# Performance work log

Hardware: AMD Instinct MI355X
Metric: run time of the kernel (lower is better)

Reference implementation:

```python
import jax, jax.numpy as jnp
import numpy as np

N_ATOMS = 20000
N_EDGES = 200000
C = 64
N_BASIS = 8
R_CUT = 5.0
NORM_FACTOR = 10.0
EPS = 1e-6
# coupling paths (in_way, r_way, out_way) with out = in + r - 2k, all ways <= 2
# index: 0:(0,0,0) 1:(0,1,1) 2:(0,2,2) 3:(1,0,1) 4:(1,1,0) 5:(1,1,2) 6:(1,2,1) 7:(2,0,2) 8:(2,1,1) 9:(2,2,0) 10:(2,2,2)
N_COMBO = 11


def setup_inputs() -> dict:
    key = jax.random.key(0)
    ks = jax.random.split(key, 16)
    f32 = jnp.float32
    return {
        "node0": jax.random.normal(ks[0], (N_ATOMS, C), f32),
        "node1": jax.random.normal(ks[1], (N_ATOMS, C, 3), f32),
        "node2": jax.random.normal(ks[2], (N_ATOMS, C, 3, 3), f32),
        "edge0": jax.random.normal(ks[3], (N_EDGES, C), f32),
        "rij": jax.random.normal(ks[4], (N_EDGES, 3), f32),
        "idx_i": jax.random.randint(ks[5], (N_EDGES,), 0, N_ATOMS),
        "idx_j": jax.random.randint(ks[6], (N_EDGES,), 0, N_ATOMS),
        "rbf_w": jax.random.normal(ks[7], (N_COMBO, N_BASIS, C), f32) * 0.1,
        "si_w0": jax.random.normal(ks[8], (C, C), f32) / np.sqrt(C),
        "si_b0": jnp.zeros((C,), f32),
        "si_w1": jax.random.normal(ks[9], (C, C), f32) / np.sqrt(C),
        "si_w2": jax.random.normal(ks[10], (C, C), f32) / np.sqrt(C),
        "nl_w1": jax.random.normal(ks[11], (C,), f32) * 0.1,
        "nl_b1": jnp.zeros((C,), f32),
        "nl_w2": jax.random.normal(ks[12], (C,), f32) * 0.1,
        "nl_b2": jnp.zeros((C,), f32),
    }


def reference(node0, node1, node2, edge0, rij, rbf_w, si_w0, si_b0, si_w1, si_w2,
              nl_w1, nl_b1, nl_w2, nl_b2, idx_i, idx_j):
    # ---- radial filters: Gaussian RBF * cosine cutoff, mixed per coupling path ----
    d = jnp.linalg.norm(rij, axis=-1)                         # [E]
    rhat = rij / (d[:, None] + 1e-12)                          # [E,3]
    mu = jnp.linspace(0.0, R_CUT, N_BASIS)
    g = jnp.exp(-2.0 * (d[:, None] - mu) ** 2)                 # [E,B]
    fcut = 0.5 * (jnp.cos(jnp.pi * jnp.clip(d, 0.0, R_CUT) / R_CUT) + 1.0)
    rbf = g * fcut[:, None]                                    # [E,B]
    fc = jnp.einsum('eb,kbc->kec', rbf, rbf_w)                 # [K,E,C]
    # ---- filter tensors of r_way 1,2 (outer products of unit vector) ----
    T1 = rhat                                                  # [E,3]
    T2 = rhat[:, :, None] * rhat[:, None, :]                   # [E,3,3]
    # ---- GraphConvLayer (conv_mode='node_j'): gather neighbor features ----
    h0 = node0[idx_j]                                          # [E,C]
    h1 = node1[idx_j]                                          # [E,C,3]
    h2 = node2[idx_j]                                          # [E,C,3,3]
    m0 = (fc[0] * h0
          + fc[4] * jnp.einsum('ecx,ex->ec', h1, T1)
          + fc[9] * jnp.einsum('ecxy,exy->ec', h2, T2))
    m1 = (fc[1][:, :, None] * (h0[:, :, None] * T1[:, None, :])
          + fc[3][:, :, None] * h1
          + fc[6][:, :, None] * jnp.einsum('ecx,exy->ecy', h1, T2)
          + fc[8][:, :, None] * jnp.einsum('ecxy,ey->ecx', h2, T1))
    m2 = (fc[2][:, :, None, None] * (h0[:, :, None, None] * T2[:, None])
          + fc[5][:, :, None, None] * (h1[:, :, :, None] * T1[:, None, None, :])
          + fc[7][:, :, None, None] * h2
          + fc[10][:, :, None, None] * jnp.einsum('ecxy,eyz->ecxz', h2, T2))
    # ---- per-way scatter_add over idx_i, normalized ----
    n = node0.shape[0]
    a0 = jax.ops.segment_sum(m0, idx_i, num_segments=n) / NORM_FACTOR
    a1 = jax.ops.segment_sum(m1, idx_i, num_segments=n) / NORM_FACTOR
    a2 = jax.ops.segment_sum(m2, idx_i, num_segments=n) / NORM_FACTOR
    # ---- SelfInteractionLayer: per-way channel mixing (bias only for way 0) ----
    s0 = a0 @ si_w0 + si_b0
    s1 = jnp.einsum('ncx,cd->ndx', a1, si_w1)
    s2 = jnp.einsum('ncxy,cd->ndxy', a2, si_w2)
    # ---- NonLinearLayer: silu on scalars, norm-gated silu on higher ways ----
    r0 = jax.nn.silu(s0)
    nrm1 = jnp.sqrt(jnp.sum(s1 * s1, axis=-1) + EPS)
    r1 = s1 * jax.nn.silu(nrm1 * nl_w1 + nl_b1)[:, :, None]
    nrm2 = jnp.sqrt(jnp.sum(s2 * s2, axis=(-2, -1)) + EPS)
    r2 = s2 * jax.nn.silu(nrm2 * nl_w2 + nl_b2)[:, :, None, None]
    # ---- res_add with node_info; update_edge=False -> edge_info unchanged ----
    return (node0 + r0, node1 + r1, node2 + r2, edge0)
```

## Files before the change

### kernel.cpp

```cpp
#include <hip/hip_runtime.h>
#include <math.h>

#define N_ATOMS 20000
#define N_EDGES 200000
#define CH 64
#define NB 8
#define NK 11
#define COPY_BLOCKS 12500

__global__ __launch_bounds__(256) void hist_kernel(
    const int* __restrict__ idx_i, int* __restrict__ counts)
{
    int e = blockIdx.x * blockDim.x + threadIdx.x;
    if (e >= N_EDGES) return;
    atomicAdd(&counts[idx_i[e]], 1);
}

__global__ __launch_bounds__(1024) void scan_kernel(
    const int* __restrict__ counts, int* __restrict__ offsets,
    int* __restrict__ cursor)
{
    __shared__ int part[1024];
    const int CHUNK = 20;
    int t = threadIdx.x;
    int beg = t * CHUNK;
    int s = 0;
    for (int k = 0; k < CHUNK; ++k) {
        int idx = beg + k;
        if (idx < N_ATOMS) s += counts[idx];
    }
    part[t] = s;
    __syncthreads();
    for (int off = 1; off < 1024; off <<= 1) {
        int v = (t >= off) ? part[t - off] : 0;
        __syncthreads();
        part[t] += v;
        __syncthreads();
    }
    int run = part[t] - s;
    for (int k = 0; k < CHUNK; ++k) {
        int idx = beg + k;
        if (idx < N_ATOMS) {
            offsets[idx] = run;
            cursor[idx] = run;
            run += counts[idx];
        }
    }
    if (t == 0) offsets[N_ATOMS] = N_EDGES;
}

__global__ __launch_bounds__(256) void scatter_geom_kernel(
    const float* __restrict__ rij, const int* __restrict__ idx_i,
    const int* __restrict__ idx_j, int* __restrict__ cursor,
    int* __restrict__ jlist, float4* __restrict__ ge4)
{
    int e = blockIdx.x * blockDim.x + threadIdx.x;
    if (e >= N_EDGES) return;

    float rx = rij[e * 3 + 0];
    float ry = rij[e * 3 + 1];
    float rz = rij[e * 3 + 2];
    float d = sqrtf(rx * rx + ry * ry + rz * rz);
    float inv = 1.0f / (d + 1e-12f);

    float dc = fminf(d, 5.0f);
    float fcut = 0.5f * (cosf(3.14159265358979323846f * dc * 0.2f) + 1.0f);

    float rbf[NB];
#pragma unroll
    for (int b = 0; b < NB; ++b) {
        float mu = (5.0f / 7.0f) * (float)b;
        float t = d - mu;
        rbf[b] = expf(-2.0f * t * t) * fcut;
    }

    int p = atomicAdd(&cursor[idx_i[e]], 1);
    jlist[p] = idx_j[e];
    ge4[p * 3 + 0] = make_float4(rx * inv, ry * inv, rz * inv, rbf[0]);
    ge4[p * 3 + 1] = make_float4(rbf[1], rbf[2], rbf[3], rbf[4]);
    ge4[p * 3 + 2] = make_float4(rbf[5], rbf[6], rbf[7], 0.f);
}

__global__ __launch_bounds__(64, 2) void atom_fused_kernel(
    const float* __restrict__ node0, const float* __restrict__ node1,
    const float* __restrict__ node2,
    const int* __restrict__ jlist, const int* __restrict__ offsets,
    const float4* __restrict__ ge4, const float* __restrict__ rbf_w,
    const float* __restrict__ si_w0, const float* __restrict__ si_b0,
    const float* __restrict__ si_w1, const float* __restrict__ si_w2,
    const float* __restrict__ nl_w1, const float* __restrict__ nl_b1,
    const float* __restrict__ nl_w2, const float* __restrict__ nl_b2,
    float* __restrict__ out0, float* __restrict__ out1, float* __restrict__ out2,
    const float4* __restrict__ edge0_in, float4* __restrict__ edge0_out)
{
    int n = blockIdx.x;
    int c = threadIdx.x;

    if (n >= N_ATOMS) {
        int cb = n - N_ATOMS;
        size_t base = (size_t)cb * 256;
#pragma unroll
        for (int k = 0; k < 4; ++k)
            edge0_out[base + k * 64 + c] = edge0_in[base + k * 64 + c];
        return;
    }

    __shared__ float abuf[CH][13];

    float wreg[NK * NB];
#pragma unroll
    for (int kb = 0; kb < NK * NB; ++kb) wreg[kb] = rbf_w[kb * CH + c];

    float a0 = 0.f;
    float a1[3] = {0.f, 0.f, 0.f};
    float a2[9] = {0.f, 0.f, 0.f, 0.f, 0.f, 0.f, 0.f, 0.f, 0.f};

    int beg = offsets[n];
    int end = offsets[n + 1];

    float4 g0, g1v, g2v;
    float h0 = 0.f, h1[3] = {0.f, 0.f, 0.f};
    float h2[9] = {0.f, 0.f, 0.f, 0.f, 0.f, 0.f, 0.f, 0.f, 0.f};
    int jnx = 0;

    if (beg < end) {
        int j = jlist[beg];
        g0 = ge4[beg * 3 + 0];
        g1v = ge4[beg * 3 + 1];
        g2v = ge4[beg * 3 + 2];
        h0 = node0[(size_t)j * CH + c];
#pragma unroll
        for (int x = 0; x < 3; ++x) h1[x] = node1[((size_t)j * CH + c) * 3 + x];
#pragma unroll
        for (int q = 0; q < 9; ++q) h2[q] = node2[((size_t)j * CH + c) * 9 + q];
        jnx = (beg + 1 < end) ? jlist[beg + 1] : 0;
    }

    for (int p = beg; p < end; ++p) {
        float rh[3] = {g0.x, g0.y, g0.z};
        float rbf[NB] = {g0.w, g1v.x, g1v.y, g1v.z, g1v.w, g2v.x, g2v.y, g2v.z};
        float ch0 = h0;
        float ch1[3] = {h1[0], h1[1], h1[2]};
        float ch2[9];
#pragma unroll
        for (int q = 0; q < 9; ++q) ch2[q] = h2[q];

        if (p + 1 < end) {
            int j2 = jnx;
            g0 = ge4[(p + 1) * 3 + 0];
            g1v = ge4[(p + 1) * 3 + 1];
            g2v = ge4[(p + 1) * 3 + 2];
            h0 = node0[(size_t)j2 * CH + c];
#pragma unroll
            for (int x = 0; x < 3; ++x) h1[x] = node1[((size_t)j2 * CH + c) * 3 + x];
#pragma unroll
            for (int q = 0; q < 9; ++q) h2[q] = node2[((size_t)j2 * CH + c) * 9 + q];
            jnx = (p + 2 < end) ? jlist[p + 2] : 0;
        }

        float fc[NK];
#pragma unroll
        for (int k = 0; k < NK; ++k) {
            float s = 0.f;
#pragma unroll
            for (int b = 0; b < NB; ++b) s = fmaf(rbf[b], wreg[k * NB + b], s);
            fc[k] = s;
        }

        float u1 = ch1[0] * rh[0] + ch1[1] * rh[1] + ch1[2] * rh[2];
        float v2[3];
#pragma unroll
        for (int x = 0; x < 3; ++x)
            v2[x] = ch2[x * 3] * rh[0] + ch2[x * 3 + 1] * rh[1] + ch2[x * 3 + 2] * rh[2];
        float w2 = v2[0] * rh[0] + v2[1] * rh[1] + v2[2] * rh[2];

        a0 = fmaf(fc[0], ch0, a0);
        a0 = fmaf(fc[4], u1, a0);
        a0 = fmaf(fc[9], w2, a0);

        float c1 = fc[1] * ch0 + fc[6] * u1;
#pragma unroll
        for (int x = 0; x < 3; ++x)
            a1[x] += c1 * rh[x] + fc[3] * ch1[x] + fc[8] * v2[x];

#pragma unroll
        for (int x = 0; x < 3; ++x) {
            float cx = fc[2] * ch0 * rh[x] + fc[5] * ch1[x] + fc[10] * v2[x];
#pragma unroll
            for (int y = 0; y < 3; ++y)
                a2[x * 3 + y] += cx * rh[y] + fc[7] * ch2[x * 3 + y];
        }
    }

    const float SC = 0.1f;
    abuf[c][0] = a0 * SC;
#pragma unroll
    for (int x = 0; x < 3; ++x) abuf[c][1 + x] = a1[x] * SC;
#pragma unroll
    for (int q = 0; q < 9; ++q) abuf[c][4 + q] = a2[q] * SC;

    __syncthreads();

    int d = c;
    float s0 = si_b0[d];
    float s1[3] = {0.f, 0.f, 0.f};
    float s2[9] = {0.f, 0.f, 0.f, 0.f, 0.f, 0.f, 0.f, 0.f, 0.f};

#pragma unroll 4
    for (int cc = 0; cc < CH; ++cc) {
        float w0 = si_w0[cc * CH + d];
        float w1 = si_w1[cc * CH + d];
        float w2m = si_w2[cc * CH + d];
        const float* a = abuf[cc];
        s0 = fmaf(a[0], w0, s0);
#pragma unroll
        for (int x = 0; x < 3; ++x) s1[x] = fmaf(a[1 + x], w1, s1[x]);
#pragma unroll
        for (int q = 0; q < 9; ++q) s2[q] = fmaf(a[4 + q], w2m, s2[q]);
    }

    float r0 = s0 / (1.0f + expf(-s0));

    float n1 = sqrtf(s1[0] * s1[0] + s1[1] * s1[1] + s1[2] * s1[2] + 1e-6f);
    float g1 = n1 * nl_w1[d] + nl_b1[d];
    float gate1 = g1 / (1.0f + expf(-g1));

    float n2sq = 1e-6f;
#pragma unroll
    for (int q = 0; q < 9; ++q) n2sq = fmaf(s2[q], s2[q], n2sq);
    float n2 = sqrtf(n2sq);
    float g2 = n2 * nl_w2[d] + nl_b2[d];
    float gate2 = g2 / (1.0f + expf(-g2));

    out0[(size_t)n * CH + d] = node0[(size_t)n * CH + d] + r0;
#pragma unroll
    for (int x = 0; x < 3; ++x)
        out1[((size_t)n * CH + d) * 3 + x] =
            node1[((size_t)n * CH + d) * 3 + x] + s1[x] * gate1;
#pragma unroll
    for (int q = 0; q < 9; ++q)
        out2[((size_t)n * CH + d) * 9 + q] =
            node2[((size_t)n * CH + d) * 9 + q] + s2[q] * gate2;
}

extern "C" void kernel_launch(void* const* d_in, const int* in_sizes, int n_in,
                              void* d_out, int out_size, void* d_ws, size_t ws_size,
                              hipStream_t stream) {
    const float* node0 = (const float*)d_in[0];
    const float* node1 = (const float*)d_in[1];
    const float* node2 = (const float*)d_in[2];
    const float* edge0 = (const float*)d_in[3];
    const float* rij   = (const float*)d_in[4];
    const int*   idx_i = (const int*)d_in[5];
    const int*   idx_j = (const int*)d_in[6];
    const float* rbf_w = (const float*)d_in[7];
    const float* si_w0 = (const float*)d_in[8];
    const float* si_b0 = (const float*)d_in[9];
    const float* si_w1 = (const float*)d_in[10];
    const float* si_w2 = (const float*)d_in[11];
    const float* nl_w1 = (const float*)d_in[12];
    const float* nl_b1 = (const float*)d_in[13];
    const float* nl_w2 = (const float*)d_in[14];
    const float* nl_b2 = (const float*)d_in[15];

    float* out = (float*)d_out;
    float* out0 = out;
    float* out1 = out + (size_t)N_ATOMS * CH;
    float* out2 = out1 + (size_t)N_ATOMS * CH * 3;
    float* oute = out2 + (size_t)N_ATOMS * CH * 9;

    char* ws = (char*)d_ws;
    int* counts  = (int*)ws;                              ws += N_ATOMS * sizeof(int);
    int* cursor  = (int*)ws;                              ws += N_ATOMS * sizeof(int);
    int* offsets = (int*)ws;                              ws += (N_ATOMS + 1) * sizeof(int);
    ws = (char*)(((size_t)ws + 15) & ~(size_t)15);
    int* jlist   = (int*)ws;                              ws += N_EDGES * sizeof(int);
    ws = (char*)(((size_t)ws + 15) & ~(size_t)15);
    float4* ge4  = (float4*)ws;

    hipMemsetAsync(counts, 0, N_ATOMS * sizeof(int), stream);

    hist_kernel<<<(N_EDGES + 255) / 256, 256, 0, stream>>>(idx_i, counts);

    scan_kernel<<<1, 1024, 0, stream>>>(counts, offsets, cursor);

    scatter_geom_kernel<<<(N_EDGES + 255) / 256, 256, 0, stream>>>(
        rij, idx_i, idx_j, cursor, jlist, ge4);

    atom_fused_kernel<<<N_ATOMS + COPY_BLOCKS, 64, 0, stream>>>(
        node0, node1, node2, jlist, offsets, ge4, rbf_w,
        si_w0, si_b0, si_w1, si_w2, nl_w1, nl_b1, nl_w2, nl_b2,
        out0, out1, out2,
        (const float4*)edge0, (float4*)oute);
}
```

Baseline: 210.1 us.

## Split per-atom accumulation across four wavefronts by output component

```diff
diff --git a/kernel.cpp b/kernel.cpp
--- a/kernel.cpp
+++ b/kernel.cpp
@@ -6,7 +6,7 @@
 #define CH 64
 #define NB 8
 #define NK 11
-#define COPY_BLOCKS 12500
+#define COPY_BLOCKS 3125
 
 __global__ __launch_bounds__(256) void hist_kernel(
     const int* __restrict__ idx_i, int* __restrict__ counts)
@@ -81,7 +81,144 @@
     ge4[p * 3 + 2] = make_float4(rbf[5], rbf[6], rbf[7], 0.f);
 }
 
-__global__ __launch_bounds__(64, 2) void atom_fused_kernel(
+template<int WID>
+__device__ __forceinline__ void accum_loop(
+    int n, int c,
+    const int* __restrict__ offsets,
+    const int* __restrict__ jlist, const float4* __restrict__ ge4,
+    const float* __restrict__ node0, const float* __restrict__ node1,
+    const float* __restrict__ node2, const float* __restrict__ rbf_w,
+    float* __restrict__ abuf)
+{
+    constexpr int NP = (WID == 0) ? 3 : 4;
+    constexpr int PTH[4][4] = {{0, 4, 9, 0}, {1, 3, 6, 8}, {2, 5, 7, 10}, {2, 5, 7, 10}};
+
+    float wp[NP][NB];
+#pragma unroll
+    for (int pi = 0; pi < NP; ++pi)
+#pragma unroll
+        for (int b = 0; b < NB; ++b)
+            wp[pi][b] = rbf_w[(PTH[WID][pi] * NB + b) * CH + c];
+
+    float acc[(WID == 2) ? 6 : (WID == 1 || WID == 3) ? 3 : 1];
+#pragma unroll
+    for (int q = 0; q < (int)(sizeof(acc) / sizeof(float)); ++q) acc[q] = 0.f;
+
+    int beg = offsets[n];
+    int end = offsets[n + 1];
+
+    auto LOADH = [&](int j, float& H0, float* H1, float* H2) {
+        size_t b0 = (size_t)j * CH + c;
+        H0 = node0[b0];
+        if constexpr (WID <= 1) {
+#pragma unroll
+            for (int x = 0; x < 3; ++x) H1[x] = node1[b0 * 3 + x];
+#pragma unroll
+            for (int q = 0; q < 9; ++q) H2[q] = node2[b0 * 9 + q];
+        } else if constexpr (WID == 2) {
+            H1[0] = node1[b0 * 3 + 0];
+            H1[1] = node1[b0 * 3 + 1];
+#pragma unroll
+            for (int q = 0; q < 6; ++q) H2[q] = node2[b0 * 9 + q];
+        } else {
+            H1[0] = node1[b0 * 3 + 2];
+#pragma unroll
+            for (int q = 0; q < 3; ++q) H2[q] = node2[b0 * 9 + 6 + q];
+        }
+    };
+
+    float4 g0, g1, g2;
+    float ch0 = 0.f, ch1[3], ch2[9];
+    int jn = 0;
+
+    if (beg < end) {
+        g0 = ge4[beg * 3 + 0];
+        g1 = ge4[beg * 3 + 1];
+        g2 = ge4[beg * 3 + 2];
+        LOADH(jlist[beg], ch0, ch1, ch2);
+        jn = (beg + 1 < end) ? jlist[beg + 1] : 0;
+    }
+
+    for (int p = beg; p < end; ++p) {
+        float rh[3] = {g0.x, g0.y, g0.z};
+        float rbf[NB] = {g0.w, g1.x, g1.y, g1.z, g1.w, g2.x, g2.y, g2.z};
+        float sh0 = ch0;
+        float sh1[3], sh2[9];
+#pragma unroll
+        for (int x = 0; x < 3; ++x) sh1[x] = ch1[x];
+#pragma unroll
+        for (int q = 0; q < 9; ++q) sh2[q] = ch2[q];
+
+        if (p + 1 < end) {
+            g0 = ge4[(p + 1) * 3 + 0];
+            g1 = ge4[(p + 1) * 3 + 1];
+            g2 = ge4[(p + 1) * 3 + 2];
+            LOADH(jn, ch0, ch1, ch2);
+            jn = (p + 2 < end) ? jlist[p + 2] : 0;
+        }
+
+        float fc[NP];
+#pragma unroll
+        for (int pi = 0; pi < NP; ++pi) {
+            float s = 0.f;
+#pragma unroll
+            for (int b = 0; b < NB; ++b) s = fmaf(rbf[b], wp[pi][b], s);
+            fc[pi] = s;
+        }
+
+        if constexpr (WID == 0) {
+            float u1 = sh1[0] * rh[0] + sh1[1] * rh[1] + sh1[2] * rh[2];
+            float v2x = sh2[0] * rh[0] + sh2[1] * rh[1] + sh2[2] * rh[2];
+            float v2y = sh2[3] * rh[0] + sh2[4] * rh[1] + sh2[5] * rh[2];
+            float v2z = sh2[6] * rh[0] + sh2[7] * rh[1] + sh2[8] * rh[2];
+            float w2 = v2x * rh[0] + v2y * rh[1] + v2z * rh[2];
+            acc[0] = fmaf(fc[0], sh0, acc[0]);
+            acc[0] = fmaf(fc[1], u1, acc[0]);
+            acc[0] = fmaf(fc[2], w2, acc[0]);
+        } else if constexpr (WID == 1) {
+            float u1 = sh1[0] * rh[0] + sh1[1] * rh[1] + sh1[2] * rh[2];
+            float v2[3];
+#pragma unroll
+            for (int x = 0; x < 3; ++x)
+                v2[x] = sh2[x * 3] * rh[0] + sh2[x * 3 + 1] * rh[1] + sh2[x * 3 + 2] * rh[2];
+            float t = fc[0] * sh0 + fc[2] * u1;
+#pragma unroll
+            for (int x = 0; x < 3; ++x)
+                acc[x] += t * rh[x] + fc[1] * sh1[x] + fc[3] * v2[x];
+        } else if constexpr (WID == 2) {
+#pragma unroll
+            for (int x = 0; x < 2; ++x) {
+                float v2x = sh2[x * 3] * rh[0] + sh2[x * 3 + 1] * rh[1] + sh2[x * 3 + 2] * rh[2];
+                float cx = fc[0] * sh0 * rh[x] + fc[1] * sh1[x] + fc[3] * v2x;
+#pragma unroll
+                for (int y = 0; y < 3; ++y)
+                    acc[x * 3 + y] += cx * rh[y] + fc[2] * sh2[x * 3 + y];
+            }
+        } else {
+            float v2z = sh2[0] * rh[0] + sh2[1] * rh[1] + sh2[2] * rh[2];
+            float cx = fc[0] * sh0 * rh[2] + fc[1] * sh1[0] + fc[3] * v2z;
+#pragma unroll
+            for (int y = 0; y < 3; ++y)
+                acc[y] += cx * rh[y] + fc[2] * sh2[y];
+        }
+    }
+
+    const float SC = 0.1f;
+    if constexpr (WID == 0) {
+        abuf[c * 16 + 0] = acc[0] * SC;
+    } else if constexpr (WID == 1) {
+#pragma unroll
+        for (int x = 0; x < 3; ++x) abuf[c * 16 + 1 + x] = acc[x] * SC;
+    } else if constexpr (WID == 2) {
+#pragma unroll
+        for (int q = 0; q < 6; ++q) abuf[c * 16 + 4 + q] = acc[q] * SC;
+    } else {
+#pragma unroll
+        for (int q = 0; q < 3; ++q) abuf[c * 16 + 10 + q] = acc[q] * SC;
+    }
+}
+
+__global__ __launch_bounds__(256, 4) void atom_fused_kernel(
     const float* __restrict__ node0, const float* __restrict__ node1,
     const float* __restrict__ node2,
     const int* __restrict__ jlist, const int* __restrict__ offsets,
@@ -94,153 +231,99 @@
     const float4* __restrict__ edge0_in, float4* __restrict__ edge0_out)
 {
     int n = blockIdx.x;
-    int c = threadIdx.x;
+    int wv = threadIdx.x >> 6;
+    int c = threadIdx.x & 63;
 
     if (n >= N_ATOMS) {
-        int cb = n - N_ATOMS;
-        size_t base = (size_t)cb * 256;
+        size_t base = (size_t)(n - N_ATOMS) * 1024;
 #pragma unroll
         for (int k = 0; k < 4; ++k)
-            edge0_out[base + k * 64 + c] = edge0_in[base + k * 64 + c];
+            edge0_out[base + k * 256 + threadIdx.x] = edge0_in[base + k * 256 + threadIdx.x];
         return;
     }
 
-    __shared__ float abuf[CH][13];
-
-    float wreg[NK * NB];
-#pragma unroll
-    for (int kb = 0; kb < NK * NB; ++kb) wreg[kb] = rbf_w[kb * CH + c];
-
-    float a0 = 0.f;
-    float a1[3] = {0.f, 0.f, 0.f};
-    float a2[9] = {0.f, 0.f, 0.f, 0.f, 0.f, 0.f, 0.f, 0.f, 0.f};
-
-    int beg = offsets[n];
-    int end = offsets[n + 1];
-
-    float4 g0, g1v, g2v;
-    float h0 = 0.f, h1[3] = {0.f, 0.f, 0.f};
-    float h2[9] = {0.f, 0.f, 0.f, 0.f, 0.f, 0.f, 0.f, 0.f, 0.f};
-    int jnx = 0;
-
-    if (beg < end) {
-        int j = jlist[beg];
-        g0 = ge4[beg * 3 + 0];
-        g1v = ge4[beg * 3 + 1];
-        g2v = ge4[beg * 3 + 2];
-        h0 = node0[(size_t)j * CH + c];
-#pragma unroll
-        for (int x = 0; x < 3; ++x) h1[x] = node1[((size_t)j * CH + c) * 3 + x];
-#pragma unroll
-        for (int q = 0; q < 9; ++q) h2[q] = node2[((size_t)j * CH + c) * 9 + q];
-        jnx = (beg + 1 < end) ? jlist[beg + 1] : 0;
-    }
-
-    for (int p = beg; p < end; ++p) {
-        float rh[3] = {g0.x, g0.y, g0.z};
-        float rbf[NB] = {g0.w, g1v.x, g1v.y, g1v.z, g1v.w, g2v.x, g2v.y, g2v.z};
-        float ch0 = h0;
-        float ch1[3] = {h1[0], h1[1], h1[2]};
-        float ch2[9];
-#pragma unroll
-        for (int q = 0; q < 9; ++q) ch2[q] = h2[q];
-
-        if (p + 1 < end) {
-            int j2 = jnx;
-            g0 = ge4[(p + 1) * 3 + 0];
-            g1v = ge4[(p + 1) * 3 + 1];
-            g2v = ge4[(p + 1) * 3 + 2];
-            h0 = node0[(size_t)j2 * CH + c];
-#pragma unroll
-            for (int x = 0; x < 3; ++x) h1[x] = node1[((size_t)j2 * CH + c) * 3 + x];
-#pragma unroll
-            for (int q = 0; q < 9; ++q) h2[q] = node2[((size_t)j2 * CH + c) * 9 + q];
-            jnx = (p + 2 < end) ? jlist[p + 2] : 0;
-        }
-
-        float fc[NK];
-#pragma unroll
-        for (int k = 0; k < NK; ++k) {
-            float s = 0.f;
-#pragma unroll
-            for (int b = 0; b < NB; ++b) s = fmaf(rbf[b], wreg[k * NB + b], s);
-            fc[k] = s;
-        }
-
-        float u1 = ch1[0] * rh[0] + ch1[1] * rh[1] + ch1[2] * rh[2];
-        float v2[3];
+    __shared__ __align__(16) float abuf[CH * 16];
+    __shared__ float pbuf[4][CH][13];
+
+    switch (wv) {
+        case 0: accum_loop<0>(n, c, offsets, jlist, ge4, node0, node1, node2, rbf_w, abuf); break;
+        case 1: accum_loop<1>(n, c, offsets, jlist, ge4, node0, node1, node2, rbf_w, abuf); break;
+        case 2: accum_loop<2>(n, c, offsets, jlist, ge4, node0, node1, node2, rbf_w, abuf); break;
+        default: accum_loop<3>(n, c, offsets, jlist, ge4, node0, node1, node2, rbf_w, abuf); break;
+    }
+    __syncthreads();
+
+    float ps[13];
+#pragma unroll
+    for (int k = 0; k < 13; ++k) ps[k] = 0.f;
+
+    for (int t = 0; t < 16; ++t) {
+        int cc = wv * 16 + t;
+        const float* ar = &abuf[cc * 16];
+        float4 A0 = *(const float4*)(ar + 0);
+        float4 A1 = *(const float4*)(ar + 4);
+        float4 A2 = *(const float4*)(ar + 8);
+        float  A3 = ar[12];
+        float w0v = si_w0[cc * CH + c];
+        float w1v = si_w1[cc * CH + c];
+        float w2v = si_w2[cc * CH + c];
+        ps[0] = fmaf(A0.x, w0v, ps[0]);
+        ps[1] = fmaf(A0.y, w1v, ps[1]);
+        ps[2] = fmaf(A0.z, w1v, ps[2]);
+        ps[3] = fmaf(A0.w, w1v, ps[3]);
+        ps[4] = fmaf(A1.x, w2v, ps[4]);
+        ps[5] = fmaf(A1.y, w2v, ps[5]);
+        ps[6] = fmaf(A1.z, w2v, ps[6]);
+        ps[7] = fmaf(A1.w, w2v, ps[7]);
+        ps[8] = fmaf(A2.x, w2v, ps[8]);
+        ps[9] = fmaf(A2.y, w2v, ps[9]);
+        ps[10] = fmaf(A2.z, w2v, ps[10]);
+        ps[11] = fmaf(A2.w, w2v, ps[11]);
+        ps[12] = fmaf(A3, w2v, ps[12]);
+    }
+#pragma unroll
+    for (int k = 0; k < 13; ++k) pbuf[wv][c][k] = ps[k];
+    __syncthreads();
+
+    if (wv == 0) {
+        float s0 = si_b0[c];
+        float s1[3] = {0.f, 0.f, 0.f};
+#pragma unroll
+        for (int w = 0; w < 4; ++w) {
+            s0 += pbuf[w][c][0];
+#pragma unroll
+            for (int x = 0; x < 3; ++x) s1[x] += pbuf[w][c][1 + x];
+        }
+        float r0 = s0 / (1.0f + expf(-s0));
+        out0[(size_t)n * CH + c] = node0[(size_t)n * CH + c] + r0;
+
+        float n1 = sqrtf(s1[0] * s1[0] + s1[1] * s1[1] + s1[2] * s1[2] + 1e-6f);
+        float g1 = n1 * nl_w1[c] + nl_b1[c];
+        float gate1 = g1 / (1.0f + expf(-g1));
 #pragma unroll
         for (int x = 0; x < 3; ++x)
-            v2[x] = ch2[x * 3] * rh[0] + ch2[x * 3 + 1] * rh[1] + ch2[x * 3 + 2] * rh[2];
-        float w2 = v2[0] * rh[0] + v2[1] * rh[1] + v2[2] * rh[2];
-
-        a0 = fmaf(fc[0], ch0, a0);
-        a0 = fmaf(fc[4], u1, a0);
-        a0 = fmaf(fc[9], w2, a0);
-
-        float c1 = fc[1] * ch0 + fc[6] * u1;
-#pragma unroll
-        for (int x = 0; x < 3; ++x)
-            a1[x] += c1 * rh[x] + fc[3] * ch1[x] + fc[8] * v2[x];
-
-#pragma unroll
-        for (int x = 0; x < 3; ++x) {
-            float cx = fc[2] * ch0 * rh[x] + fc[5] * ch1[x] + fc[10] * v2[x];
-#pragma unroll
-            for (int y = 0; y < 3; ++y)
-                a2[x * 3 + y] += cx * rh[y] + fc[7] * ch2[x * 3 + y];
-        }
-    }
-
-    const float SC = 0.1f;
-    abuf[c][0] = a0 * SC;
-#pragma unroll
-    for (int x = 0; x < 3; ++x) abuf[c][1 + x] = a1[x] * SC;
-#pragma unroll
-    for (int q = 0; q < 9; ++q) abuf[c][4 + q] = a2[q] * SC;
-
-    __syncthreads();
-
-    int d = c;
-    float s0 = si_b0[d];
-    float s1[3] = {0.f, 0.f, 0.f};
-    float s2[9] = {0.f, 0.f, 0.f, 0.f, 0.f, 0.f, 0.f, 0.f, 0.f};
-
-#pragma unroll 4
-    for (int cc = 0; cc < CH; ++cc) {
-        float w0 = si_w0[cc * CH + d];
-        float w1 = si_w1[cc * CH + d];
-        float w2m = si_w2[cc * CH + d];
-        const float* a = abuf[cc];
-        s0 = fmaf(a[0], w0, s0);
-#pragma unroll
-        for (int x = 0; x < 3; ++x) s1[x] = fmaf(a[1 + x], w1, s1[x]);
-#pragma unroll
-        for (int q = 0; q < 9; ++q) s2[q] = fmaf(a[4 + q], w2m, s2[q]);
-    }
-
-    float r0 = s0 / (1.0f + expf(-s0));
-
-    float n1 = sqrtf(s1[0] * s1[0] + s1[1] * s1[1] + s1[2] * s1[2] + 1e-6f);
-    float g1 = n1 * nl_w1[d] + nl_b1[d];
-    float gate1 = g1 / (1.0f + expf(-g1));
-
-    float n2sq = 1e-6f;
-#pragma unroll
-    for (int q = 0; q < 9; ++q) n2sq = fmaf(s2[q], s2[q], n2sq);
-    float n2 = sqrtf(n2sq);
-    float g2 = n2 * nl_w2[d] + nl_b2[d];
-    float gate2 = g2 / (1.0f + expf(-g2));
-
-    out0[(size_t)n * CH + d] = node0[(size_t)n * CH + d] + r0;
-#pragma unroll
-    for (int x = 0; x < 3; ++x)
-        out1[((size_t)n * CH + d) * 3 + x] =
-            node1[((size_t)n * CH + d) * 3 + x] + s1[x] * gate1;
-#pragma unroll
-    for (int q = 0; q < 9; ++q)
-        out2[((size_t)n * CH + d) * 9 + q] =
-            node2[((size_t)n * CH + d) * 9 + q] + s2[q] * gate2;
+            out1[((size_t)n * CH + c) * 3 + x] =
+                node1[((size_t)n * CH + c) * 3 + x] + s1[x] * gate1;
+    } else if (wv == 1) {
+        float s2[9];
+#pragma unroll
+        for (int q = 0; q < 9; ++q) s2[q] = 0.f;
+#pragma unroll
+        for (int w = 0; w < 4; ++w)
+#pragma unroll
+            for (int q = 0; q < 9; ++q) s2[q] += pbuf[w][c][4 + q];
+
+        float n2sq = 1e-6f;
+#pragma unroll
+        for (int q = 0; q < 9; ++q) n2sq = fmaf(s2[q], s2[q], n2sq);
+        float n2 = sqrtf(n2sq);
+        float g2 = n2 * nl_w2[c] + nl_b2[c];
+        float gate2 = g2 / (1.0f + expf(-g2));
+#pragma unroll
+        for (int q = 0; q < 9; ++q)
+            out2[((size_t)n * CH + c) * 9 + q] =
+                node2[((size_t)n * CH + c) * 9 + q] + s2[q] * gate2;
+    }
 }
 
 extern "C" void kernel_launch(void* const* d_in, const int* in_sizes, int n_in,
@@ -287,7 +370,7 @@
     scatter_geom_kernel<<<(N_EDGES + 255) / 256, 256, 0, stream>>>(
         rij, idx_i, idx_j, cursor, jlist, ge4);
 
-    atom_fused_kernel<<<N_ATOMS + COPY_BLOCKS, 64, 0, stream>>>(
+    atom_fused_kernel<<<N_ATOMS + COPY_BLOCKS, 256, 0, stream>>>(
         node0, node1, node2, jlist, offsets, ge4, rbf_w,
         si_w0, si_b0, si_w1, si_w2, nl_w1, nl_b1, nl_w2, nl_b2,
         out0, out1, out2,
```

New measurement: 277.4 us. 32.1% more time.

## Pack four atoms per block and move RBF weights from registers to LDS

Applied to the files above, without the earlier changes.

```diff
diff --git a/kernel.cpp b/kernel.cpp
--- a/kernel.cpp
+++ b/kernel.cpp
@@ -6,7 +6,11 @@
 #define CH 64
 #define NB 8
 #define NK 11
-#define COPY_BLOCKS 12500
+#define ATOMS_PER_BLOCK 4
+#define ATOM_BLOCKS (N_ATOMS / ATOMS_PER_BLOCK)
+#define COPY_F4 (N_EDGES * CH / 4)
+#define COPY_PER_BLOCK 1024
+#define COPY_BLOCKS (COPY_F4 / COPY_PER_BLOCK)
 
 __global__ __launch_bounds__(256) void hist_kernel(
     const int* __restrict__ idx_i, int* __restrict__ counts)
@@ -81,7 +85,7 @@
     ge4[p * 3 + 2] = make_float4(rbf[5], rbf[6], rbf[7], 0.f);
 }
 
-__global__ __launch_bounds__(64, 2) void atom_fused_kernel(
+__global__ __launch_bounds__(256) void atom_fused_kernel(
     const float* __restrict__ node0, const float* __restrict__ node1,
     const float* __restrict__ node2,
     const int* __restrict__ jlist, const int* __restrict__ offsets,
@@ -93,23 +97,27 @@
     float* __restrict__ out0, float* __restrict__ out1, float* __restrict__ out2,
     const float4* __restrict__ edge0_in, float4* __restrict__ edge0_out)
 {
-    int n = blockIdx.x;
-    int c = threadIdx.x;
-
-    if (n >= N_ATOMS) {
-        int cb = n - N_ATOMS;
-        size_t base = (size_t)cb * 256;
+    int bid = blockIdx.x;
+
+    if (bid >= ATOM_BLOCKS) {
+        size_t base = (size_t)(bid - ATOM_BLOCKS) * COPY_PER_BLOCK;
 #pragma unroll
         for (int k = 0; k < 4; ++k)
-            edge0_out[base + k * 64 + c] = edge0_in[base + k * 64 + c];
+            edge0_out[base + k * 256 + threadIdx.x] =
+                edge0_in[base + k * 256 + threadIdx.x];
         return;
     }
 
-    __shared__ float abuf[CH][13];
-
-    float wreg[NK * NB];
-#pragma unroll
-    for (int kb = 0; kb < NK * NB; ++kb) wreg[kb] = rbf_w[kb * CH + c];
+    __shared__ float wlds[NK * NB * CH];
+    __shared__ float2 ab2[ATOMS_PER_BLOCK][CH][7];
+
+    for (int t = threadIdx.x; t < NK * NB * CH; t += 256)
+        wlds[t] = rbf_w[t];
+    __syncthreads();
+
+    int wv = threadIdx.x >> 6;
+    int c = threadIdx.x & 63;
+    int n = bid * ATOMS_PER_BLOCK + wv;
 
     float a0 = 0.f;
     float a1[3] = {0.f, 0.f, 0.f};
@@ -158,12 +166,17 @@
             jnx = (p + 2 < end) ? jlist[p + 2] : 0;
         }
 
+        int cop = c;
+        asm volatile("" : "+v"(cop));
+        const float* wl = &wlds[cop];
+
         float fc[NK];
 #pragma unroll
         for (int k = 0; k < NK; ++k) {
             float s = 0.f;
 #pragma unroll
-            for (int b = 0; b < NB; ++b) s = fmaf(rbf[b], wreg[k * NB + b], s);
+            for (int b = 0; b < NB; ++b)
+                s = fmaf(rbf[b], wl[(k * NB + b) * CH], s);
             fc[k] = s;
         }
 
@@ -193,54 +206,68 @@
     }
 
     const float SC = 0.1f;
-    abuf[c][0] = a0 * SC;
-#pragma unroll
-    for (int x = 0; x < 3; ++x) abuf[c][1 + x] = a1[x] * SC;
-#pragma unroll
-    for (int q = 0; q < 9; ++q) abuf[c][4 + q] = a2[q] * SC;
-
-    __syncthreads();
-
-    int d = c;
-    float s0 = si_b0[d];
+    ab2[wv][c][0] = make_float2(a0 * SC, a1[0] * SC);
+    ab2[wv][c][1] = make_float2(a1[1] * SC, a1[2] * SC);
+    ab2[wv][c][2] = make_float2(a2[0] * SC, a2[1] * SC);
+    ab2[wv][c][3] = make_float2(a2[2] * SC, a2[3] * SC);
+    ab2[wv][c][4] = make_float2(a2[4] * SC, a2[5] * SC);
+    ab2[wv][c][5] = make_float2(a2[6] * SC, a2[7] * SC);
+    ab2[wv][c][6] = make_float2(a2[8] * SC, 0.f);
+
+    __builtin_amdgcn_wave_barrier();
+
+    float s0 = si_b0[c];
     float s1[3] = {0.f, 0.f, 0.f};
     float s2[9] = {0.f, 0.f, 0.f, 0.f, 0.f, 0.f, 0.f, 0.f, 0.f};
 
-#pragma unroll 4
     for (int cc = 0; cc < CH; ++cc) {
-        float w0 = si_w0[cc * CH + d];
-        float w1 = si_w1[cc * CH + d];
-        float w2m = si_w2[cc * CH + d];
-        const float* a = abuf[cc];
-        s0 = fmaf(a[0], w0, s0);
-#pragma unroll
-        for (int x = 0; x < 3; ++x) s1[x] = fmaf(a[1 + x], w1, s1[x]);
-#pragma unroll
-        for (int q = 0; q < 9; ++q) s2[q] = fmaf(a[4 + q], w2m, s2[q]);
+        float2 q0 = ab2[wv][cc][0];
+        float2 q1 = ab2[wv][cc][1];
+        float2 q2 = ab2[wv][cc][2];
+        float2 q3 = ab2[wv][cc][3];
+        float2 q4 = ab2[wv][cc][4];
+        float2 q5 = ab2[wv][cc][5];
+        float2 q6 = ab2[wv][cc][6];
+        float w0 = si_w0[cc * CH + c];
+        float w1 = si_w1[cc * CH + c];
+        float w2m = si_w2[cc * CH + c];
+        s0 = fmaf(q0.x, w0, s0);
+        s1[0] = fmaf(q0.y, w1, s1[0]);
+        s1[1] = fmaf(q1.x, w1, s1[1]);
+        s1[2] = fmaf(q1.y, w1, s1[2]);
+        s2[0] = fmaf(q2.x, w2m, s2[0]);
+        s2[1] = fmaf(q2.y, w2m, s2[1]);
+        s2[2] = fmaf(q3.x, w2m, s2[2]);
+        s2[3] = fmaf(q3.y, w2m, s2[3]);
+        s2[4] = fmaf(q4.x, w2m, s2[4]);
+        s2[5] = fmaf(q4.y, w2m, s2[5]);
+        s2[6] = fmaf(q5.x, w2m, s2[6]);
+        s2[7] = fmaf(q5.y, w2m, s2[7]);
+        s2[8] = fmaf(q6.x, w2m, s2[8]);
     }
 
     float r0 = s0 / (1.0f + expf(-s0));
 
     float n1 = sqrtf(s1[0] * s1[0] + s1[1] * s1[1] + s1[2] * s1[2] + 1e-6f);
-    float g1 = n1 * nl_w1[d] + nl_b1[d];
+    float g1 = n1 * nl_w1[c] + nl_b1[c];
     float gate1 = g1 / (1.0f + expf(-g1));
 
     float n2sq = 1e-6f;
 #pragma unroll
     for (int q = 0; q < 9; ++q) n2sq = fmaf(s2[q], s2[q], n2sq);
     float n2 = sqrtf(n2sq);
-    float g2 = n2 * nl_w2[d] + nl_b2[d];
+    float g2 = n2 * nl_w2[c] + nl_b2[c];
     float gate2 = g2 / (1.0f + expf(-g2));
 
-    out0[(size_t)n * CH + d] = node0[(size_t)n * CH + d] + r0;
+    out0[(size_t)n * CH + c] = node0[(size_t)n * CH + c] + r0;
 #pragma unroll
     for (int x = 0; x < 3; ++x)
-        out1[((size_t)n * CH + d) * 3 + x] =
-            node1[((size_t)n * CH + d) * 3 + x] + s1[x] * gate1;
+        out1[((size_t)n * CH + c) * 3 + x] =
+            node1[((size_t)n * CH + c) * 3 + x] + s1[x] * gate1;
 #pragma unroll
     for (int q = 0; q < 9; ++q)
-        out2[((size_t)n * CH + d) * 9 + q] =
-            node2[((size_t)n * CH + d) * 9 + q] + s2[q] * gate2;
+        out2[((size_t)n * CH + c) * 9 + q] =
+            node2[((size_t)n * CH + c) * 9 + q] + s2[q] * gate2;
 }
 
 extern "C" void kernel_launch(void* const* d_in, const int* in_sizes, int n_in,
@@ -287,7 +314,7 @@
     scatter_geom_kernel<<<(N_EDGES + 255) / 256, 256, 0, stream>>>(
         rij, idx_i, idx_j, cursor, jlist, ge4);
 
-    atom_fused_kernel<<<N_ATOMS + COPY_BLOCKS, 64, 0, stream>>>(
+    atom_fused_kernel<<<ATOM_BLOCKS + COPY_BLOCKS, 256, 0, stream>>>(
         node0, node1, node2, jlist, offsets, ge4, rbf_w,
         si_w0, si_b0, si_w1, si_w2, nl_w1, nl_b1, nl_w2, nl_b2,
         out0, out1, out2,
```

Measured after the change: 244.1 us. 1.16x slower.
